# Performance work log

Measured on AMD Instinct MI355X. Metric: run time of the kernel, lower is better.

## Reference

```python
import jax, jax.numpy as jnp
import numpy as np

N = 262144   # total atoms across all images
D = 128      # fingerprint (input_dimension)
H = 128      # hidden width (hiddenlayers = (128, 128))
S = 4        # number of unique element symbols (experts)
B = 1024     # number of images (segments)


def setup_inputs() -> dict:
    key = jax.random.key(0)
    ks = jax.random.split(key, 10)
    x = jax.random.normal(ks[0], (N, D), dtype=jnp.float32)
    symbol_ids = jax.random.randint(ks[1], (N,), 0, S, dtype=jnp.int32)
    image_ids = jnp.sort(jax.random.randint(ks[2], (N,), 0, B, dtype=jnp.int32))
    # per-symbol MLP params (xavier-ish scaling)
    W1 = jax.random.normal(ks[3], (S, D, H), dtype=jnp.float32) / np.sqrt(D)
    b1 = jnp.zeros((S, H), dtype=jnp.float32)
    W2 = jax.random.normal(ks[4], (S, H, H), dtype=jnp.float32) / np.sqrt(H)
    b2 = jnp.zeros((S, H), dtype=jnp.float32)
    W3 = jax.random.normal(ks[5], (S, H), dtype=jnp.float32) / np.sqrt(H)
    b3 = jnp.zeros((S,), dtype=jnp.float32)
    # per-symbol affine energy scale/shift
    slope = 1.0 + 0.1 * jax.random.normal(ks[6], (S,), dtype=jnp.float32)
    intercept = 0.1 * jax.random.normal(ks[7], (S,), dtype=jnp.float32)
    return {
        "x": x, "W1": W1, "b1": b1, "W2": W2, "b2": b2, "W3": W3, "b3": b3,
        "slope": slope, "intercept": intercept,
        "symbol_ids": symbol_ids, "image_ids": image_ids,
    }


def reference(x, W1, b1, W2, b2, W3, b3, slope, intercept, symbol_ids, image_ids):
    # Run every atom through every symbol's tiny MLP (S small), then select.
    h = jax.nn.relu(jnp.einsum('nd,sdh->nsh', x, W1) + b1)          # [N,S,H]
    h = jax.nn.relu(jnp.einsum('nsh,shk->nsk', h, W2) + b2)         # [N,S,H]
    e = jnp.einsum('nsh,sh->ns', h, W3) + b3                         # [N,S] atomic energy per expert
    e = slope * e + intercept                                        # per-symbol affine
    e_atom = jnp.take_along_axis(e, symbol_ids[:, None].astype(jnp.int32), axis=1)[:, 0]  # [N] routed
    # per-image energy = sum of atomic energies in that image
    return jax.ops.segment_sum(e_atom, image_ids, num_segments=B)    # [B]
```

## Files before the change

kernel.cpp:

```cpp
#include <hip/hip_runtime.h>
#include <hip/hip_bf16.h>
#include <stdint.h>

typedef _Float16 f16x8 __attribute__((ext_vector_type(8)));
typedef float f32x4 __attribute__((ext_vector_type(4)));
typedef unsigned int u32x4 __attribute__((ext_vector_type(4)));

#define N_ATOMS 262144
#define NSYM 4
#define NIMG 1024

__global__ void hist_kernel(const int* __restrict__ sym, int* __restrict__ wbh) {
  int b = blockIdx.x;
  int i = b * 256 + threadIdx.x;
  int lane = threadIdx.x & 63, wave = threadIdx.x >> 6;
  __shared__ int wcnt[4][NSYM];
  int s = sym[i];
#pragma unroll
  for (int t = 0; t < NSYM; ++t) {
    unsigned long long m = __ballot(s == t);
    if (lane == 0) wcnt[wave][t] = __popcll(m);
  }
  __syncthreads();
  if (threadIdx.x < NSYM)
    wbh[b * 4 + threadIdx.x] = wcnt[0][threadIdx.x] + wcnt[1][threadIdx.x] +
                               wcnt[2][threadIdx.x] + wcnt[3][threadIdx.x];
}

__global__ void offsets_kernel(const int* __restrict__ wbh, int* __restrict__ bases,
                               int* __restrict__ offs, int* __restrict__ perm) {
  __shared__ int wtot[4][NSYM];
  __shared__ int offsh[NSYM + 1];
  __shared__ int totsh[NSYM];
  int t = threadIdx.x, lane = t & 63, wave = t >> 6;
  int pre[4][NSYM];
  int sum[NSYM] = {0, 0, 0, 0};
#pragma unroll
  for (int k = 0; k < 4; ++k)
#pragma unroll
    for (int s2 = 0; s2 < NSYM; ++s2) {
      pre[k][s2] = sum[s2];
      sum[s2] += wbh[(t * 4 + k) * 4 + s2];
    }
  int inc[NSYM] = {sum[0], sum[1], sum[2], sum[3]};
  for (int d = 1; d < 64; d <<= 1) {
#pragma unroll
    for (int s2 = 0; s2 < NSYM; ++s2) {
      int v = __shfl_up(inc[s2], d);
      if (lane >= d) inc[s2] += v;
    }
  }
  if (lane == 63)
#pragma unroll
    for (int s2 = 0; s2 < NSYM; ++s2) wtot[wave][s2] = inc[s2];
  __syncthreads();
  int wb[NSYM];
#pragma unroll
  for (int s2 = 0; s2 < NSYM; ++s2) {
    wb[s2] = 0;
    for (int w = 0; w < wave; ++w) wb[s2] += wtot[w][s2];
  }
  if (t == 255)
#pragma unroll
    for (int s2 = 0; s2 < NSYM; ++s2) totsh[s2] = wb[s2] + inc[s2];
  __syncthreads();
  if (t == 0) {
    int o = 0;
    offsh[0] = 0; offs[0] = 0;
    for (int s2 = 0; s2 < NSYM; ++s2) {
      o += (totsh[s2] + 255) & ~255;
      offsh[s2 + 1] = o; offs[s2 + 1] = o;
    }
  }
  __syncthreads();
#pragma unroll
  for (int k = 0; k < 4; ++k)
#pragma unroll
    for (int s2 = 0; s2 < NSYM; ++s2)
      bases[(t * 4 + k) * 4 + s2] = offsh[s2] + wb[s2] + (inc[s2] - sum[s2]) + pre[k][s2];
  for (int s2 = 0; s2 < NSYM; ++s2) {
    int lo = offsh[s2] + totsh[s2], hi = offsh[s2 + 1];
    for (int i = lo + t; i < hi; i += 256) perm[i] = -1;
  }
}

__global__ void scatter_kernel(const int* __restrict__ sym, const int* __restrict__ bases,
                               int* __restrict__ perm) {
  int b = blockIdx.x;
  int i = b * 256 + threadIdx.x;
  int lane = threadIdx.x & 63, wave = threadIdx.x >> 6;
  __shared__ int wcnt[4][NSYM];
  int s = sym[i];
  unsigned long long mymask = 0;
#pragma unroll
  for (int t = 0; t < NSYM; ++t) {
    unsigned long long m = __ballot(s == t);
    if (lane == 0) wcnt[wave][t] = __popcll(m);
    if (s == t) mymask = m;
  }
  __syncthreads();
  int off = bases[b * 4 + s];
  for (int w = 0; w < wave; ++w) off += wcnt[w][s];
  off += __popcll(mymask & ((1ull << lane) - 1ull));
  perm[off] = i;
}

__global__ void wconv_kernel(const float* __restrict__ W1, const float* __restrict__ W2,
                             unsigned short* __restrict__ wt) {
  int idx = blockIdx.x * 256 + threadIdx.x;
  int t = idx >> 14;
  int layer = t >> 2, s = t & 3;
  int rem = idx & 16383;
  int h = rem >> 7, u = rem & 127;
  int gs = u >> 3, j = u & 7;
  int d = ((gs ^ (h & 7)) << 3) + j;
  const float* W = layer ? W2 : W1;
  _Float16 hv = (_Float16)W[(s * 128 + d) * 128 + h];
  wt[t * 16384 + h * 128 + u] = __builtin_bit_cast(unsigned short, hv);
}

__global__ __launch_bounds__(512, 2) void mlp_gemm(
    const float* __restrict__ x, const unsigned short* __restrict__ wt,
    const int* __restrict__ perm, const int* __restrict__ offs,
    const float* __restrict__ b1, const float* __restrict__ b2,
    const float* __restrict__ W3, const float* __restrict__ b3,
    const float* __restrict__ slope, const float* __restrict__ intercept,
    float* __restrict__ e_atom) {
  extern __shared__ char lds[];

  int s = blockIdx.x >> 6;
  int kblk = blockIdx.x & 63;
  int base = offs[s];
  int T = (offs[s + 1] - base) >> 8;

  int tid = threadIdx.x;
  int wave = tid >> 6, lane = tid & 63;
  int r0 = lane & 15, chunk = lane >> 4;
  char* bounce = lds + 65536 + wave * 8192;

  const unsigned short* w1p = wt + (size_t)(0 + s) * 16384;
  const unsigned short* w2p = wt + (size_t)(4 + s) * 16384;

#pragma unroll
  for (int it = 0; it < 8; ++it) {
    int gb = it * 512 + wave * 64;
    const unsigned short* src = (gb >= 2048) ? (w2p + (size_t)(gb - 2048 + lane) * 8)
                                             : (w1p + (size_t)(gb + lane) * 8);
    __builtin_amdgcn_global_load_lds((const unsigned int*)src,
                                     (unsigned int*)(lds + (size_t)gb * 16), 16, 0, 0);
  }

  float b1v[8], b2v[8], w3v[8];
#pragma unroll
  for (int cf = 0; cf < 8; ++cf) {
    b1v[cf] = b1[s * 128 + cf * 16 + r0];
    b2v[cf] = b2[s * 128 + cf * 16 + r0];
    w3v[cf] = W3[s * 128 + cf * 16 + r0];
  }
  float sl = slope[s], ic = intercept[s], bb = b3[s];

  __syncthreads();

  f32x4 zero4 = {0.f, 0.f, 0.f, 0.f};

  for (int t = kblk; t < T; t += 64) {
    int a0 = perm[base + (t << 8) + wave * 32 + r0];
    int a1 = perm[base + (t << 8) + wave * 32 + 16 + r0];
    f16x8 ah[8];
#pragma unroll
    for (int rf = 0; rf < 2; ++rf) {
      int atom = rf ? a1 : a0;
      const float* xr = x + (long)(atom < 0 ? 0 : atom) * 128;
#pragma unroll
      for (int kk = 0; kk < 4; ++kk) {
        float4 v0 = *(const float4*)(xr + kk * 32 + chunk * 8);
        float4 v1 = *(const float4*)(xr + kk * 32 + chunk * 8 + 4);
        f16x8 f;
        f[0] = (_Float16)v0.x; f[1] = (_Float16)v0.y;
        f[2] = (_Float16)v0.z; f[3] = (_Float16)v0.w;
        f[4] = (_Float16)v1.x; f[5] = (_Float16)v1.y;
        f[6] = (_Float16)v1.z; f[7] = (_Float16)v1.w;
        ah[rf * 4 + kk] = f;
      }
    }

    f32x4 acc[2][8];
#pragma unroll
    for (int i = 0; i < 2; ++i)
#pragma unroll
      for (int j = 0; j < 8; ++j) acc[i][j] = zero4;

#pragma unroll
    for (int k = 0; k < 4; ++k)
#pragma unroll
      for (int cf = 0; cf < 8; ++cf) {
        int row = cf * 16 + r0;
        f16x8 bh = *(const f16x8*)(lds + row * 256 +
                                   ((((k * 4 + chunk)) << 4) ^ ((row & 7) << 4)));
        acc[0][cf] = __builtin_amdgcn_mfma_f32_16x16x32_f16(ah[k], bh, acc[0][cf], 0, 0, 0);
        acc[1][cf] = __builtin_amdgcn_mfma_f32_16x16x32_f16(ah[4 + k], bh, acc[1][cf], 0, 0, 0);
      }

#pragma unroll
    for (int hp2 = 0; hp2 < 2; ++hp2) {
#pragma unroll
      for (int cf4 = 0; cf4 < 4; ++cf4) {
        int cf = hp2 * 4 + cf4;
        float bias = b1v[cf];
        int colp = cf4 * 16 + r0;
#pragma unroll
        for (int rf = 0; rf < 2; ++rf)
#pragma unroll
          for (int rr = 0; rr < 4; ++rr) {
            int row = rf * 16 + chunk * 4 + rr;
            float v = fmaxf(acc[rf][cf][rr] + bias, 0.f);
            unsigned short h = __builtin_bit_cast(unsigned short, (_Float16)v);
            int cc = colp ^ (chunk << 4) ^ (rr << 2);
            *(unsigned int*)(bounce + row * 256 + cc * 4) = ((unsigned int)h << 16) | h;
          }
      }
#pragma unroll
      for (int kk2 = 0; kk2 < 2; ++kk2) {
        int kk = hp2 * 2 + kk2;
#pragma unroll
        for (int rf = 0; rf < 2; ++rf) {
          int row = rf * 16 + r0;
          int xr3 = ((r0 >> 2) << 4) ^ ((r0 & 3) << 2);
          int c0 = kk2 * 32 + chunk * 8;
          u32x4 pa = *(const u32x4*)(bounce + row * 256 + (c0 ^ xr3) * 4);
          u32x4 pb = *(const u32x4*)(bounce + row * 256 + ((c0 + 4) ^ xr3) * 4);
          unsigned int h01 = (pa[0] >> 16) | (pa[1] & 0xffff0000u);
          unsigned int h23 = (pa[2] >> 16) | (pa[3] & 0xffff0000u);
          unsigned int h45 = (pb[0] >> 16) | (pb[1] & 0xffff0000u);
          unsigned int h67 = (pb[2] >> 16) | (pb[3] & 0xffff0000u);
          u32x4 hq = {h01, h23, h45, h67};
          ah[rf * 4 + kk] = __builtin_bit_cast(f16x8, hq);
        }
      }
    }

#pragma unroll
    for (int i = 0; i < 2; ++i)
#pragma unroll
      for (int j = 0; j < 8; ++j) acc[i][j] = zero4;

#pragma unroll
    for (int k = 0; k < 4; ++k)
#pragma unroll
      for (int cf = 0; cf < 8; ++cf) {
        int row = cf * 16 + r0;
        f16x8 bh = *(const f16x8*)(lds + 32768 + row * 256 +
                                   ((((k * 4 + chunk)) << 4) ^ ((row & 7) << 4)));
        acc[0][cf] = __builtin_amdgcn_mfma_f32_16x16x32_f16(ah[k], bh, acc[0][cf], 0, 0, 0);
        acc[1][cf] = __builtin_amdgcn_mfma_f32_16x16x32_f16(ah[4 + k], bh, acc[1][cf], 0, 0, 0);
      }

    float p[2][4] = {{0.f, 0.f, 0.f, 0.f}, {0.f, 0.f, 0.f, 0.f}};
#pragma unroll
    for (int cf = 0; cf < 8; ++cf)
#pragma unroll
      for (int rf = 0; rf < 2; ++rf)
#pragma unroll
        for (int rr = 0; rr < 4; ++rr)
          p[rf][rr] += fmaxf(acc[rf][cf][rr] + b2v[cf], 0.f) * w3v[cf];
#pragma unroll
    for (int m = 1; m < 16; m <<= 1)
#pragma unroll
      for (int rf = 0; rf < 2; ++rf)
#pragma unroll
        for (int rr = 0; rr < 4; ++rr) p[rf][rr] += __shfl_xor(p[rf][rr], m);

    if (r0 == 0) {
#pragma unroll
      for (int rf = 0; rf < 2; ++rf)
#pragma unroll
        for (int rr = 0; rr < 4; ++rr) {
          int row = wave * 32 + rf * 16 + chunk * 4 + rr;
          int a = perm[base + (t << 8) + row];
          if (a >= 0) e_atom[a] = sl * (p[rf][rr] + bb) + ic;
        }
    }
  }
}

__global__ void segsum_kernel(const float* __restrict__ e_atom, const int* __restrict__ img,
                              float* __restrict__ out, int n) {
  int b = blockIdx.x;
  int lo = 0, hi = n;
  while (lo < hi) { int m = (lo + hi) >> 1; if (img[m] < b) lo = m + 1; else hi = m; }
  int lo2 = lo, hi2 = n;
  while (lo2 < hi2) { int m = (lo2 + hi2) >> 1; if (img[m] < b + 1) lo2 = m + 1; else hi2 = m; }
  float sum = 0.f;
  for (int i = lo + threadIdx.x; i < lo2; i += blockDim.x) sum += e_atom[i];
  for (int m = 32; m; m >>= 1) sum += __shfl_down(sum, m);
  __shared__ float part[4];
  int lane = threadIdx.x & 63, wave = threadIdx.x >> 6;
  if (lane == 0) part[wave] = sum;
  __syncthreads();
  if (threadIdx.x == 0) out[b] = part[0] + part[1] + part[2] + part[3];
}

extern "C" void kernel_launch(void* const* d_in, const int* in_sizes, int n_in,
                              void* d_out, int out_size, void* d_ws, size_t ws_size,
                              hipStream_t stream) {
  const float* x         = (const float*)d_in[0];
  const float* W1        = (const float*)d_in[1];
  const float* b1        = (const float*)d_in[2];
  const float* W2        = (const float*)d_in[3];
  const float* b2        = (const float*)d_in[4];
  const float* W3        = (const float*)d_in[5];
  const float* b3        = (const float*)d_in[6];
  const float* slope     = (const float*)d_in[7];
  const float* intercept = (const float*)d_in[8];
  const int* sym         = (const int*)d_in[9];
  const int* img         = (const int*)d_in[10];

  char* ws = (char*)d_ws;
  int* wbh    = (int*)ws;
  int* bases  = (int*)(ws + 16384);
  int* offs   = (int*)(ws + 32768);
  int* perm   = (int*)(ws + 32832);
  float* e_atom = (float*)(ws + 32832 + 1052672);
  unsigned short* wt = (unsigned short*)(ws + 32832 + 1052672 + 1048576);

  hist_kernel<<<1024, 256, 0, stream>>>(sym, wbh);
  offsets_kernel<<<1, 256, 0, stream>>>(wbh, bases, offs, perm);
  scatter_kernel<<<1024, 256, 0, stream>>>(sym, bases, perm);
  wconv_kernel<<<512, 256, 0, stream>>>(W1, W2, wt);
  mlp_gemm<<<256, 512, 131072, stream>>>(x, wt, perm, offs, b1, b2,
                                         W3, b3, slope, intercept, e_atom);
  segsum_kernel<<<NIMG, 256, 0, stream>>>(e_atom, img, (float*)d_out, N_ATOMS);
}
```

Measured before the change: 76.99 us.

## Pre-permute and convert x to fp16 during scatter for coalesced GEMM loads

The scatter kernel now reads x rows, converts them to fp16, and writes them in symbol-sorted order into a workspace buffer. The MLP GEMM then loads contiguous fp16 rows instead of gathering fp32 rows through perm. This removes the random gather and halves the bytes the GEMM reads, but adds a full extra pass writing a 64MB staging buffer. The path is enabled only when the workspace is large enough.

```diff
diff --git a/kernel.cpp b/kernel.cpp
--- a/kernel.cpp
+++ b/kernel.cpp
@@ -3,8 +3,10 @@
 #include <stdint.h>
 
 typedef _Float16 f16x8 __attribute__((ext_vector_type(8)));
+typedef __fp16 hf2 __attribute__((ext_vector_type(2)));
 typedef float f32x4 __attribute__((ext_vector_type(4)));
 typedef unsigned int u32x4 __attribute__((ext_vector_type(4)));
+typedef unsigned int u32x2 __attribute__((ext_vector_type(2)));
 
 #define N_ATOMS 262144
 #define NSYM 4
@@ -84,12 +86,14 @@
   }
 }
 
-__global__ void scatter_kernel(const int* __restrict__ sym, const int* __restrict__ bases,
-                               int* __restrict__ perm) {
+__global__ void scatter_kernel(const float* __restrict__ x, const int* __restrict__ sym,
+                               const int* __restrict__ bases, int* __restrict__ perm,
+                               unsigned short* __restrict__ xg, int do_cvt) {
   int b = blockIdx.x;
   int i = b * 256 + threadIdx.x;
   int lane = threadIdx.x & 63, wave = threadIdx.x >> 6;
   __shared__ int wcnt[4][NSYM];
+  __shared__ int lds_off[256];
   int s = sym[i];
   unsigned long long mymask = 0;
 #pragma unroll
@@ -103,6 +107,30 @@
   for (int w = 0; w < wave; ++w) off += wcnt[w][s];
   off += __popcll(mymask & ((1ull << lane) - 1ull));
   perm[off] = i;
+  lds_off[threadIdx.x] = off;
+  if (!do_cvt) return;
+  __syncthreads();
+
+  int l32 = lane & 31, half = lane >> 5;
+  int gbase = b * 256 + wave * 64;
+#pragma unroll
+  for (int it = 0; it < 4; ++it) {
+    float4 v[8];
+#pragma unroll
+    for (int u = 0; u < 8; ++u) {
+      int row = (it * 8 + u) * 2 + half;
+      v[u] = *(const float4*)(x + (size_t)(gbase + row) * 128 + l32 * 4);
+    }
+#pragma unroll
+    for (int u = 0; u < 8; ++u) {
+      int row = (it * 8 + u) * 2 + half;
+      int o = lds_off[wave * 64 + row];
+      hf2 p0 = __builtin_amdgcn_cvt_pkrtz(v[u].x, v[u].y);
+      hf2 p1 = __builtin_amdgcn_cvt_pkrtz(v[u].z, v[u].w);
+      u32x2 w2 = {__builtin_bit_cast(unsigned int, p0), __builtin_bit_cast(unsigned int, p1)};
+      *(u32x2*)(xg + (size_t)o * 128 + l32 * 4) = w2;
+    }
+  }
 }
 
 __global__ void wconv_kernel(const float* __restrict__ W1, const float* __restrict__ W2,
@@ -119,8 +147,10 @@
   wt[t * 16384 + h * 128 + u] = __builtin_bit_cast(unsigned short, hv);
 }
 
+template <bool COAL>
 __global__ __launch_bounds__(512, 2) void mlp_gemm(
-    const float* __restrict__ x, const unsigned short* __restrict__ wt,
+    const float* __restrict__ x, const unsigned short* __restrict__ xg,
+    const unsigned short* __restrict__ wt,
     const int* __restrict__ perm, const int* __restrict__ offs,
     const float* __restrict__ b1, const float* __restrict__ b2,
     const float* __restrict__ W3, const float* __restrict__ b3,
@@ -164,23 +194,34 @@
   f32x4 zero4 = {0.f, 0.f, 0.f, 0.f};
 
   for (int t = kblk; t < T; t += 64) {
-    int a0 = perm[base + (t << 8) + wave * 32 + r0];
-    int a1 = perm[base + (t << 8) + wave * 32 + 16 + r0];
     f16x8 ah[8];
-#pragma unroll
-    for (int rf = 0; rf < 2; ++rf) {
-      int atom = rf ? a1 : a0;
-      const float* xr = x + (long)(atom < 0 ? 0 : atom) * 128;
-#pragma unroll
-      for (int kk = 0; kk < 4; ++kk) {
-        float4 v0 = *(const float4*)(xr + kk * 32 + chunk * 8);
-        float4 v1 = *(const float4*)(xr + kk * 32 + chunk * 8 + 4);
-        f16x8 f;
-        f[0] = (_Float16)v0.x; f[1] = (_Float16)v0.y;
-        f[2] = (_Float16)v0.z; f[3] = (_Float16)v0.w;
-        f[4] = (_Float16)v1.x; f[5] = (_Float16)v1.y;
-        f[6] = (_Float16)v1.z; f[7] = (_Float16)v1.w;
-        ah[rf * 4 + kk] = f;
+    if (COAL) {
+#pragma unroll
+      for (int rf = 0; rf < 2; ++rf) {
+        const unsigned short* xr =
+            xg + (size_t)(base + (t << 8) + wave * 32 + rf * 16 + r0) * 128;
+#pragma unroll
+        for (int kk = 0; kk < 4; ++kk)
+          ah[rf * 4 + kk] = *(const f16x8*)(xr + kk * 32 + chunk * 8);
+      }
+    } else {
+      int a0 = perm[base + (t << 8) + wave * 32 + r0];
+      int a1 = perm[base + (t << 8) + wave * 32 + 16 + r0];
+#pragma unroll
+      for (int rf = 0; rf < 2; ++rf) {
+        int atom = rf ? a1 : a0;
+        const float* xr = x + (long)(atom < 0 ? 0 : atom) * 128;
+#pragma unroll
+        for (int kk = 0; kk < 4; ++kk) {
+          float4 v0 = *(const float4*)(xr + kk * 32 + chunk * 8);
+          float4 v1 = *(const float4*)(xr + kk * 32 + chunk * 8 + 4);
+          f16x8 f;
+          f[0] = (_Float16)v0.x; f[1] = (_Float16)v0.y;
+          f[2] = (_Float16)v0.z; f[3] = (_Float16)v0.w;
+          f[4] = (_Float16)v1.x; f[5] = (_Float16)v1.y;
+          f[6] = (_Float16)v1.z; f[7] = (_Float16)v1.w;
+          ah[rf * 4 + kk] = f;
+        }
       }
     }
 
@@ -321,13 +362,21 @@
   int* offs   = (int*)(ws + 32768);
   int* perm   = (int*)(ws + 32832);
   float* e_atom = (float*)(ws + 32832 + 1052672);
-  unsigned short* wt = (unsigned short*)(ws + 32832 + 1052672 + 1048576);
+  unsigned short* wt = (unsigned short*)(ws + 2134080);
+  size_t xg_off = 2396416;
+  size_t xg_bytes = (size_t)(N_ATOMS + 1024) * 256;
+  unsigned short* xg = (unsigned short*)(ws + xg_off);
+  int coal = (ws_size >= xg_off + xg_bytes) ? 1 : 0;
 
   hist_kernel<<<1024, 256, 0, stream>>>(sym, wbh);
   offsets_kernel<<<1, 256, 0, stream>>>(wbh, bases, offs, perm);
-  scatter_kernel<<<1024, 256, 0, stream>>>(sym, bases, perm);
+  scatter_kernel<<<1024, 256, 0, stream>>>(x, sym, bases, perm, xg, coal);
   wconv_kernel<<<512, 256, 0, stream>>>(W1, W2, wt);
-  mlp_gemm<<<256, 512, 131072, stream>>>(x, wt, perm, offs, b1, b2,
-                                         W3, b3, slope, intercept, e_atom);
+  if (coal)
+    mlp_gemm<true><<<256, 512, 131072, stream>>>(x, xg, wt, perm, offs, b1, b2,
+                                                 W3, b3, slope, intercept, e_atom);
+  else
+    mlp_gemm<false><<<256, 512, 131072, stream>>>(x, xg, wt, perm, offs, b1, b2,
+                                                  W3, b3, slope, intercept, e_atom);
   segsum_kernel<<<NIMG, 256, 0, stream>>>(e_atom, img, (float*)d_out, N_ATOMS);
 }
```

After: 94.31 us. +22.5%, slower.

## Software-prefetch next tile's gathered x rows into registers and stage via LDS

Applied to the files above, without the earlier changes.

The gather of x rows for the next tile is issued during layer-2 compute and held in 16 float4 registers per lane. It is then converted to fp16 with packed cvt and written through the per-wave LDS staging buffer to form the MFMA A operands. Loads are now row-contiguous (each half-wave reads one whole 512-byte row), which coalesces better than the old per-lane strided reads. Perm indices are kept in registers and broadcast by shuffle instead of being re-read from global memory at store time. The price is higher register pressure, which may cut occupancy, plus extra LDS traffic.

```diff
diff --git a/kernel.cpp b/kernel.cpp
--- a/kernel.cpp
+++ b/kernel.cpp
@@ -3,8 +3,10 @@
 #include <stdint.h>
 
 typedef _Float16 f16x8 __attribute__((ext_vector_type(8)));
+typedef __fp16 hf2 __attribute__((ext_vector_type(2)));
 typedef float f32x4 __attribute__((ext_vector_type(4)));
 typedef unsigned int u32x4 __attribute__((ext_vector_type(4)));
+typedef unsigned int u32x2 __attribute__((ext_vector_type(2)));
 
 #define N_ATOMS 262144
 #define NSYM 4
@@ -136,7 +138,8 @@
   int tid = threadIdx.x;
   int wave = tid >> 6, lane = tid & 63;
   int r0 = lane & 15, chunk = lane >> 4;
-  char* bounce = lds + 65536 + wave * 8192;
+  int l32 = lane & 31, half = lane >> 5;
+  char* stage = lds + 65536 + wave * 8192;
 
   const unsigned short* w1p = wt + (size_t)(0 + s) * 16384;
   const unsigned short* w2p = wt + (size_t)(4 + s) * 16384;
@@ -159,30 +162,41 @@
   }
   float sl = slope[s], ic = intercept[s], bb = b3[s];
 
+  int cur_perm = (kblk < T) ? perm[base + (kblk << 8) + wave * 32 + l32] : -1;
+  float4 raw[16];
+#pragma unroll
+  for (int it = 0; it < 16; ++it) {
+    int atom = __shfl(cur_perm, it * 2 + half);
+    raw[it] = *(const float4*)(x + (size_t)(atom < 0 ? 0 : atom) * 128 + l32 * 4);
+  }
+
   __syncthreads();
 
   f32x4 zero4 = {0.f, 0.f, 0.f, 0.f};
 
   for (int t = kblk; t < T; t += 64) {
-    int a0 = perm[base + (t << 8) + wave * 32 + r0];
-    int a1 = perm[base + (t << 8) + wave * 32 + 16 + r0];
+    int tn = t + 64;
+    int nperm = -1;
+    if (tn < T) nperm = perm[base + (tn << 8) + wave * 32 + l32];
+
+#pragma unroll
+    for (int it = 0; it < 16; ++it) {
+      int row = it * 2 + half;
+      hf2 p0 = __builtin_amdgcn_cvt_pkrtz(raw[it].x, raw[it].y);
+      hf2 p1 = __builtin_amdgcn_cvt_pkrtz(raw[it].z, raw[it].w);
+      u32x2 w2 = {__builtin_bit_cast(unsigned int, p0), __builtin_bit_cast(unsigned int, p1)};
+      int gs = (l32 >> 1) ^ (row & 7);
+      *(u32x2*)(stage + row * 256 + gs * 16 + (l32 & 1) * 8) = w2;
+    }
     f16x8 ah[8];
 #pragma unroll
-    for (int rf = 0; rf < 2; ++rf) {
-      int atom = rf ? a1 : a0;
-      const float* xr = x + (long)(atom < 0 ? 0 : atom) * 128;
+    for (int rf = 0; rf < 2; ++rf)
 #pragma unroll
       for (int kk = 0; kk < 4; ++kk) {
-        float4 v0 = *(const float4*)(xr + kk * 32 + chunk * 8);
-        float4 v1 = *(const float4*)(xr + kk * 32 + chunk * 8 + 4);
-        f16x8 f;
-        f[0] = (_Float16)v0.x; f[1] = (_Float16)v0.y;
-        f[2] = (_Float16)v0.z; f[3] = (_Float16)v0.w;
-        f[4] = (_Float16)v1.x; f[5] = (_Float16)v1.y;
-        f[6] = (_Float16)v1.z; f[7] = (_Float16)v1.w;
-        ah[rf * 4 + kk] = f;
-      }
-    }
+        int row = rf * 16 + r0;
+        ah[rf * 4 + kk] = *(const f16x8*)(stage + row * 256 +
+                                          (((kk * 4 + chunk) ^ (row & 7)) << 4));
+      }
 
     f32x4 acc[2][8];
 #pragma unroll
@@ -216,7 +230,7 @@
             float v = fmaxf(acc[rf][cf][rr] + bias, 0.f);
             unsigned short h = __builtin_bit_cast(unsigned short, (_Float16)v);
             int cc = colp ^ (chunk << 4) ^ (rr << 2);
-            *(unsigned int*)(bounce + row * 256 + cc * 4) = ((unsigned int)h << 16) | h;
+            *(unsigned int*)(stage + row * 256 + cc * 4) = ((unsigned int)h << 16) | h;
           }
       }
 #pragma unroll
@@ -227,8 +241,8 @@
           int row = rf * 16 + r0;
           int xr3 = ((r0 >> 2) << 4) ^ ((r0 & 3) << 2);
           int c0 = kk2 * 32 + chunk * 8;
-          u32x4 pa = *(const u32x4*)(bounce + row * 256 + (c0 ^ xr3) * 4);
-          u32x4 pb = *(const u32x4*)(bounce + row * 256 + ((c0 + 4) ^ xr3) * 4);
+          u32x4 pa = *(const u32x4*)(stage + row * 256 + (c0 ^ xr3) * 4);
+          u32x4 pb = *(const u32x4*)(stage + row * 256 + ((c0 + 4) ^ xr3) * 4);
           unsigned int h01 = (pa[0] >> 16) | (pa[1] & 0xffff0000u);
           unsigned int h23 = (pa[2] >> 16) | (pa[3] & 0xffff0000u);
           unsigned int h45 = (pb[0] >> 16) | (pb[1] & 0xffff0000u);
@@ -239,6 +253,14 @@
       }
     }
 
+    if (tn < T) {
+#pragma unroll
+      for (int it = 0; it < 16; ++it) {
+        int atom = __shfl(nperm, it * 2 + half);
+        raw[it] = *(const float4*)(x + (size_t)(atom < 0 ? 0 : atom) * 128 + l32 * 4);
+      }
+    }
+
 #pragma unroll
     for (int i = 0; i < 2; ++i)
 #pragma unroll
@@ -270,16 +292,23 @@
 #pragma unroll
         for (int rr = 0; rr < 4; ++rr) p[rf][rr] += __shfl_xor(p[rf][rr], m);
 
+    int atom_w[2][4];
+#pragma unroll
+    for (int rf = 0; rf < 2; ++rf)
+#pragma unroll
+      for (int rr = 0; rr < 4; ++rr)
+        atom_w[rf][rr] = __shfl(cur_perm, rf * 16 + chunk * 4 + rr);
+
     if (r0 == 0) {
 #pragma unroll
       for (int rf = 0; rf < 2; ++rf)
 #pragma unroll
-        for (int rr = 0; rr < 4; ++rr) {
-          int row = wave * 32 + rf * 16 + chunk * 4 + rr;
-          int a = perm[base + (t << 8) + row];
-          if (a >= 0) e_atom[a] = sl * (p[rf][rr] + bb) + ic;
-        }
-    }
+        for (int rr = 0; rr < 4; ++rr)
+          if (atom_w[rf][rr] >= 0)
+            e_atom[atom_w[rf][rr]] = sl * (p[rf][rr] + bb) + ic;
+    }
+
+    cur_perm = nperm;
   }
 }
 
@@ -321,7 +350,7 @@
   int* offs   = (int*)(ws + 32768);
   int* perm   = (int*)(ws + 32832);
   float* e_atom = (float*)(ws + 32832 + 1052672);
-  unsigned short* wt = (unsigned short*)(ws + 32832 + 1052672 + 1048576);
+  unsigned short* wt = (unsigned short*)(ws + 2134080);
 
   hist_kernel<<<1024, 256, 0, stream>>>(sym, wbh);
   offsets_kernel<<<1, 256, 0, stream>>>(wbh, bases, offs, perm);
```

New measurement: 64.89 us. 15.7% less time.
